# Optimization experiments

Hardware: AMD Instinct MI355X
Metric: run time of the kernel (lower is better)

The kernel has to match this reference:

```python
import jax, jax.numpy as jnp
import numpy as np

N = 50000; E = 1000000; H = 64; HEADS = 4; D = 16; IN = 8; ED = 4; B = 512; EMB = 128; L = 3


def _ln(x, g, b, eps=1e-5):
    mu = jnp.mean(x, axis=-1, keepdims=True)
    var = jnp.mean((x - mu) ** 2, axis=-1, keepdims=True)
    return (x - mu) / jnp.sqrt(var + eps) * g + b


def setup_inputs() -> dict:
    key = jax.random.key(0)
    ks = jax.random.split(key, 24)
    rn = lambda k, s, sc=0.05: jax.random.normal(k, s, jnp.float32) * sc
    return {
        'x': rn(ks[0], (N, IN), 1.0),
        'edge_attr': rn(ks[1], (E, ED), 1.0),
        'edge_index': jax.random.randint(ks[2], (2, E), 0, N),
        'batch': jnp.sort(jax.random.randint(ks[3], (N,), 0, B)),
        'W_in': rn(ks[4], (IN, H)), 'b_in': jnp.zeros(H, jnp.float32),
        'ln1_g': jnp.ones((L, H), jnp.float32), 'ln1_b': jnp.zeros((L, H), jnp.float32),
        'Wq': rn(ks[5], (L, H, H)), 'bq': jnp.zeros((L, H), jnp.float32),
        'Wk': rn(ks[6], (L, H, H)), 'bk': jnp.zeros((L, H), jnp.float32),
        'Wv': rn(ks[7], (L, H, H)), 'bv': jnp.zeros((L, H), jnp.float32),
        'We': rn(ks[8], (L, ED, H)),
        'Wskip': rn(ks[9], (L, H, H)), 'bskip': jnp.zeros((L, H), jnp.float32),
        'Wbeta': rn(ks[10], (L, 3 * H, 1)),
        'ln2_g': jnp.ones((L, H), jnp.float32), 'ln2_b': jnp.zeros((L, H), jnp.float32),
        'W1': rn(ks[11], (L, H, 2 * H)), 'b1': jnp.zeros((L, 2 * H), jnp.float32),
        'W2': rn(ks[12], (L, 2 * H, H)), 'b2': jnp.zeros((L, H), jnp.float32),
        'Wo1': rn(ks[13], (H, EMB)), 'bo1': jnp.zeros(EMB, jnp.float32),
        'Wo2': rn(ks[14], (EMB, EMB)), 'bo2': jnp.zeros(EMB, jnp.float32),
    }


def _forward(x, edge_attr, edge_index, batch, W_in, b_in, ln1_g, ln1_b, Wq, bq, Wk, bk, Wv, bv,
             We, Wskip, bskip, Wbeta, ln2_g, ln2_b, W1, b1, W2, b2, Wo1, bo1, Wo2, bo2):
    src, dst = edge_index[0], edge_index[1]  # message j->i aggregated at dst
    scale = 1.0 / jnp.sqrt(jnp.float32(D))
    x = x @ W_in + b_in  # [N,H]
    for l in range(L):
        xin = x
        h = _ln(x, ln1_g[l], ln1_b[l])
        q = (h @ Wq[l] + bq[l]).reshape(N, HEADS, D)
        k = (h @ Wk[l] + bk[l]).reshape(N, HEADS, D)
        v = (h @ Wv[l] + bv[l]).reshape(N, HEADS, D)
        e = (edge_attr @ We[l]).reshape(E, HEADS, D)
        k_e = k[src] + e  # [E,heads,D]
        v_e = v[src] + e
        s = jnp.sum(q[dst] * k_e, axis=-1) * scale  # [E,heads]
        m = jax.ops.segment_max(s, dst, num_segments=N)  # scatter-softmax max
        m = jnp.where(jnp.isfinite(m), m, 0.0)
        p = jnp.exp(s - m[dst])
        denom = jax.ops.segment_sum(p, dst, num_segments=N)
        alpha = p / (denom[dst] + 1e-16)
        out = jax.ops.segment_sum(alpha[:, :, None] * v_e, dst, num_segments=N).reshape(N, H)
        x_r = h @ Wskip[l] + bskip[l]
        beta = jax.nn.sigmoid(jnp.concatenate([out, x_r, out - x_r], axis=-1) @ Wbeta[l])
        out = beta * x_r + (1.0 - beta) * out
        x = xin + out  # dropout disabled (eval)
        xin = x
        h = _ln(x, ln2_g[l], ln2_b[l])
        h = jax.nn.gelu(h @ W1[l] + b1[l], approximate=False) @ W2[l] + b2[l]
        x = xin + h
    pooled = jax.ops.segment_max(x, batch, num_segments=B)  # global_max_pool
    pooled = jnp.where(jnp.isfinite(pooled), pooled, 0.0)
    emb = jax.nn.relu(pooled @ Wo1 + bo1) @ Wo2 + bo2
    norm = jnp.sqrt(jnp.sum(emb * emb, axis=-1, keepdims=True))
    return emb / jnp.maximum(norm, 1e-12)


def reference(x, edge_attr, edge_index, batch, W_in, b_in, ln1_g, ln1_b, Wq, bq, Wk, bk, Wv, bv,
              We, Wskip, bskip, Wbeta, ln2_g, ln2_b, W1, b1, W2, b2, Wo1, bo1, Wo2, bo2):
    return _forward(x, edge_attr, edge_index, batch, W_in, b_in, ln1_g, ln1_b, Wq, bq, Wk, bk,
                    Wv, bv, We, Wskip, bskip, Wbeta, ln2_g, ln2_b, W1, b1, W2, b2, Wo1, bo1, Wo2, bo2)
```

## Files before the change

kernel.cpp:

```cpp
#include <hip/hip_runtime.h>
#include <hip/hip_bf16.h>
#include <hip/hip_fp16.h>

#define Nn 50000
#define Ee 1000000
#define Bb 512
#define NG 3125
#define SCB 196

typedef unsigned short u16;
typedef unsigned int u32;
typedef _Float16 f16;
typedef _Float16 f16x8 __attribute__((ext_vector_type(8)));
typedef float f32x4 __attribute__((ext_vector_type(4)));

__device__ __forceinline__ u16 f2h(float f) { return __half_as_ushort(__float2half(f)); }
__device__ __forceinline__ float h2f_lo(u32 kv) { return __half2float(__ushort_as_half((u16)(kv & 0xffff))); }
__device__ __forceinline__ float h2f_hi(u32 kv) { return __half2float(__ushort_as_half((u16)(kv >> 16))); }

__device__ __forceinline__ float fexp2(float x) {
    float r;
    asm("v_exp_f32 %0, %1" : "=v"(r) : "v"(x));
    return r;
}

__device__ __forceinline__ float red16(float x) {
    int t;
    t = __builtin_amdgcn_update_dpp(0, __float_as_int(x), 0xB1, 0xF, 0xF, true);
    x += __int_as_float(t);
    t = __builtin_amdgcn_update_dpp(0, __float_as_int(x), 0x4E, 0xF, 0xF, true);
    x += __int_as_float(t);
    t = __builtin_amdgcn_update_dpp(0, __float_as_int(x), 0x141, 0xF, 0xF, true);
    x += __int_as_float(t);
    t = __builtin_amdgcn_update_dpp(0, __float_as_int(x), 0x140, 0xF, 0xF, true);
    x += __int_as_float(t);
    return x;
}

__global__ __launch_bounds__(256) void k_input_proj(const float* __restrict__ x,
    const float* __restrict__ Win, const float* __restrict__ bin, float* __restrict__ X)
{
    __shared__ float W[8][64];
    __shared__ float bsh[64];
    int t = threadIdx.x;
    if (t < 64) bsh[t] = bin[t];
    for (int i = t; i < 512; i += 256) W[i >> 6][i & 63] = Win[i];
    __syncthreads();
    int gid = blockIdx.x * 256 + t;
    int n = gid >> 6, c = gid & 63;
    const float* xr = x + n * 8;
    float acc = bsh[c];
#pragma unroll
    for (int k = 0; k < 8; ++k) acc = fmaf(xr[k], W[k][c], acc);
    X[gid] = acc;
}

__global__ __launch_bounds__(256) void k_hist(const int* __restrict__ ei, int* __restrict__ deg)
{
    int e = blockIdx.x * 256 + threadIdx.x;
    if (e < Ee) atomicAdd(&deg[ei[Ee + e]], 1);
}

__global__ __launch_bounds__(256) void k_part(const int* __restrict__ deg, int* __restrict__ psum)
{
    __shared__ int ws[4];
    int b = blockIdx.x, t = threadIdx.x;
    int idx = b * 256 + t;
    int v = (idx < Nn) ? deg[idx] : 0;
    int r = v;
#pragma unroll
    for (int off = 32; off; off >>= 1) r += __shfl_xor(r, off);
    if ((t & 63) == 0) ws[t >> 6] = r;
    __syncthreads();
    if (t == 0) psum[b] = ws[0] + ws[1] + ws[2] + ws[3];
}

__global__ __launch_bounds__(256) void k_scanp(const int* __restrict__ psum, int* __restrict__ poff)
{
    __shared__ int ws[4];
    int t = threadIdx.x, lane = t & 63, w = t >> 6;
    int v = (t < SCB) ? psum[t] : 0;
    int s = v;
#pragma unroll
    for (int off = 1; off < 64; off <<= 1) {
        int u = __shfl_up(s, off);
        if (lane >= off) s += u;
    }
    if (lane == 63) ws[w] = s;
    __syncthreads();
    if (t == 0) { int a = 0; for (int i = 0; i < 4; ++i) { a += ws[i]; ws[i] = a; } }
    __syncthreads();
    int incl = s + (w ? ws[w - 1] : 0);
    if (t < SCB) poff[t] = incl - v;
}

__global__ __launch_bounds__(256) void k_apply(const int* __restrict__ deg, const int* __restrict__ poff,
    int* __restrict__ rowptr)
{
    __shared__ int ws[4];
    int b = blockIdx.x, t = threadIdx.x, lane = t & 63, w = t >> 6;
    int idx = b * 256 + t;
    int v = (idx < Nn) ? deg[idx] : 0;
    int s = v;
#pragma unroll
    for (int off = 1; off < 64; off <<= 1) {
        int u = __shfl_up(s, off);
        if (lane >= off) s += u;
    }
    if (lane == 63) ws[w] = s;
    __syncthreads();
    if (t == 0) { int a = 0; for (int i = 0; i < 4; ++i) { a += ws[i]; ws[i] = a; } }
    __syncthreads();
    int incl = s + (w ? ws[w - 1] : 0) + poff[b];
    if (idx < Nn) rowptr[idx + 1] = incl;
    if (b == 0 && t == 0) rowptr[0] = 0;
}

__global__ __launch_bounds__(256) void k_scatter(const int* __restrict__ ei, const float* __restrict__ eattr,
    const int* __restrict__ rowptr, int* __restrict__ cursor, int* __restrict__ colsrc,
    float4* __restrict__ ea4)
{
    int e = blockIdx.x * 256 + threadIdx.x;
    if (e >= Ee) return;
    int d = ei[Ee + e];
    int pos = rowptr[d] + atomicAdd(&cursor[d], 1);
    colsrc[pos] = ei[e];
    ea4[pos] = *(const float4*)(eattr + (size_t)e * 4);
}

__device__ __forceinline__ f16x8 load_bfrag(const float* __restrict__ W, int NC, int col, int k0)
{
    f16x8 b;
    const float* wp = W + (size_t)k0 * NC + col;
#pragma unroll
    for (int i = 0; i < 8; ++i) b[i] = (f16)wp[i * NC];
    return b;
}

__device__ __forceinline__ void build_ln_a(const float* __restrict__ X, int n0, int lane,
    const float* __restrict__ lng, const float* __restrict__ lnb, f16x8* a)
{
    const int r = lane & 15, c = lane >> 4;
    const float* xp = X + (size_t)(n0 + r) * 64 + c * 8;
    float4 x0 = *(const float4*)(xp);
    float4 x1 = *(const float4*)(xp + 4);
    float4 x2 = *(const float4*)(xp + 32);
    float4 x3 = *(const float4*)(xp + 36);
    float xs[16] = {x0.x, x0.y, x0.z, x0.w, x1.x, x1.y, x1.z, x1.w,
                    x2.x, x2.y, x2.z, x2.w, x3.x, x3.y, x3.z, x3.w};
    float s = 0.f, s2 = 0.f;
#pragma unroll
    for (int i = 0; i < 16; ++i) { s += xs[i]; s2 = fmaf(xs[i], xs[i], s2); }
    s += __shfl_xor(s, 16);  s += __shfl_xor(s, 32);
    s2 += __shfl_xor(s2, 16); s2 += __shfl_xor(s2, 32);
    float mu = s * 0.015625f;
    float var = s2 * 0.015625f - mu * mu;
    float rstd = rsqrtf(fmaxf(var, 0.f) + 1e-5f);
    const float* gp = lng + c * 8;
    const float* bp = lnb + c * 8;
    float4 g0 = *(const float4*)(gp),      g1 = *(const float4*)(gp + 4);
    float4 g2 = *(const float4*)(gp + 32), g3 = *(const float4*)(gp + 36);
    float4 b0 = *(const float4*)(bp),      b1 = *(const float4*)(bp + 4);
    float4 b2 = *(const float4*)(bp + 32), b3 = *(const float4*)(bp + 36);
    float gs[16] = {g0.x, g0.y, g0.z, g0.w, g1.x, g1.y, g1.z, g1.w,
                    g2.x, g2.y, g2.z, g2.w, g3.x, g3.y, g3.z, g3.w};
    float bs[16] = {b0.x, b0.y, b0.z, b0.w, b1.x, b1.y, b1.z, b1.w,
                    b2.x, b2.y, b2.z, b2.w, b3.x, b3.y, b3.z, b3.w};
#pragma unroll
    for (int i = 0; i < 16; ++i) {
        float h = (xs[i] - mu) * rstd * gs[i] + bs[i];
        a[i >> 3][i & 7] = (f16)h;
    }
}

__global__ __launch_bounds__(256) void k_proj_kv(const float* __restrict__ X, u32* __restrict__ KV,
    const float* __restrict__ Wk, const float* __restrict__ Wv,
    const float* __restrict__ bk, const float* __restrict__ bv,
    const float* __restrict__ lng, const float* __restrict__ lnb)
{
    const int lane = threadIdx.x & 63;
    const int wid = (blockIdx.x * 256 + threadIdx.x) >> 6;
    const int nw = gridDim.x * 4;
    const int ch_base = lane & 15;
    const int k0b = (lane >> 4) * 8;
    f16x8 bw[8][2];
#pragma unroll
    for (int t = 0; t < 4; ++t)
#pragma unroll
        for (int s = 0; s < 2; ++s) {
            bw[t][s]     = load_bfrag(Wk, 64, t * 16 + ch_base, s * 32 + k0b);
            bw[t + 4][s] = load_bfrag(Wv, 64, t * 16 + ch_base, s * 32 + k0b);
        }
    float bk_l[4], bv_l[4];
#pragma unroll
    for (int t = 0; t < 4; ++t) { bk_l[t] = bk[t * 16 + ch_base]; bv_l[t] = bv[t * 16 + ch_base]; }
    for (int g = wid; g < NG; g += nw) {
        int n0 = g * 16;
        f16x8 a[2];
        build_ln_a(X, n0, lane, lng, lnb, a);
        f32x4 acc[8];
#pragma unroll
        for (int t = 0; t < 8; ++t) { acc[t][0] = 0.f; acc[t][1] = 0.f; acc[t][2] = 0.f; acc[t][3] = 0.f; }
#pragma unroll
        for (int t = 0; t < 8; ++t)
#pragma unroll
            for (int s = 0; s < 2; ++s)
                acc[t] = __builtin_amdgcn_mfma_f32_16x16x32_f16(a[s], bw[t][s], acc[t], 0, 0, 0);
        int rbase = n0 + (lane >> 4) * 4;
#pragma unroll
        for (int t = 0; t < 4; ++t) {
            int ch = t * 16 + ch_base;
#pragma unroll
            for (int j = 0; j < 4; ++j) {
                u32 lo = f2h(acc[t][j] + bk_l[t]);
                u32 hi = f2h(acc[t + 4][j] + bv_l[t]);
                KV[(size_t)(rbase + j) * 64 + ch] = (hi << 16) | lo;
            }
        }
    }
}

__global__ __launch_bounds__(256) void k_proj_qs(const float* __restrict__ X, float* __restrict__ QX,
    const float* __restrict__ Wq, const float* __restrict__ Ws,
    const float* __restrict__ bq, const float* __restrict__ bs_,
    const float* __restrict__ lng, const float* __restrict__ lnb)
{
    const int lane = threadIdx.x & 63;
    const int wid = (blockIdx.x * 256 + threadIdx.x) >> 6;
    const int nw = gridDim.x * 4;
    const int ch_base = lane & 15;
    const int k0b = (lane >> 4) * 8;
    f16x8 bw[8][2];
#pragma unroll
    for (int t = 0; t < 4; ++t)
#pragma unroll
        for (int s = 0; s < 2; ++s) {
            bw[t][s]     = load_bfrag(Wq, 64, t * 16 + ch_base, s * 32 + k0b);
            bw[t + 4][s] = load_bfrag(Ws, 64, t * 16 + ch_base, s * 32 + k0b);
        }
    float bq_l[4], bs_l[4];
#pragma unroll
    for (int t = 0; t < 4; ++t) { bq_l[t] = bq[t * 16 + ch_base]; bs_l[t] = bs_[t * 16 + ch_base]; }
    for (int g = wid; g < NG; g += nw) {
        int n0 = g * 16;
        f16x8 a[2];
        build_ln_a(X, n0, lane, lng, lnb, a);
        f32x4 acc[8];
#pragma unroll
        for (int t = 0; t < 8; ++t) { acc[t][0] = 0.f; acc[t][1] = 0.f; acc[t][2] = 0.f; acc[t][3] = 0.f; }
#pragma unroll
        for (int t = 0; t < 8; ++t)
#pragma unroll
            for (int s = 0; s < 2; ++s)
                acc[t] = __builtin_amdgcn_mfma_f32_16x16x32_f16(a[s], bw[t][s], acc[t], 0, 0, 0);
        int rbase = n0 + (lane >> 4) * 4;
#pragma unroll
        for (int t = 0; t < 4; ++t) {
            int ch = t * 16 + ch_base;
#pragma unroll
            for (int j = 0; j < 4; ++j) {
                float* dst = QX + (size_t)(rbase + j) * 128;
                dst[ch] = acc[t][j] + bq_l[t];
                dst[64 + ch] = acc[t + 4][j] + bs_l[t];
            }
        }
    }
}

__global__ __launch_bounds__(256) void k_edge(
    const float* __restrict__ QX, const u32* __restrict__ KV, float* __restrict__ X,
    const int* __restrict__ rowptr, const int* __restrict__ colsrc,
    const float4* __restrict__ ea4,
    const float* __restrict__ We, const float* __restrict__ Wbeta)
{
    const float SCL = 0.25f * 1.4426950408889634f;
    int lane = threadIdx.x & 63;
    int node = blockIdx.x * 4 + (threadIdx.x >> 6);
    if (node >= Nn) return;
    float we0 = We[lane], we1 = We[64 + lane];
    float we2 = We[128 + lane], we3 = We[192 + lane];
    float wbA = Wbeta[lane] + Wbeta[128 + lane];
    float wbB = Wbeta[64 + lane] - Wbeta[128 + lane];
    const float* qrow = QX + (size_t)node * 128;
    float q = qrow[lane] * SCL;
    float xr = qrow[64 + lane];
    int jb = rowptr[node], je = rowptr[node + 1];
    float l0 = 0.f, l1 = 0.f, a0 = 0.f, a1 = 0.f;
    int j = jb;
    for (; j + 3 < je; j += 4) {
        int src[4]; float4 eb[4]; u32 kv[4];
#pragma unroll
        for (int c = 0; c < 4; ++c) src[c] = colsrc[j + c];
#pragma unroll
        for (int c = 0; c < 4; ++c) kv[c] = KV[(src[c] << 6) | lane];
#pragma unroll
        for (int c = 0; c < 4; ++c) eb[c] = ea4[j + c];
        float pe[4], ve[4];
#pragma unroll
        for (int c = 0; c < 4; ++c) {
            float e = we0 * eb[c].x;
            e = fmaf(we1, eb[c].y, e); e = fmaf(we2, eb[c].z, e); e = fmaf(we3, eb[c].w, e);
            float ke = h2f_lo(kv[c]) + e;
            ve[c] = h2f_hi(kv[c]) + e;
            float p = red16(q * ke);
            pe[c] = fexp2(p);
        }
        l0 += pe[0]; l1 += pe[1];
        a0 = fmaf(pe[0], ve[0], a0); a1 = fmaf(pe[1], ve[1], a1);
        l0 += pe[2]; l1 += pe[3];
        a0 = fmaf(pe[2], ve[2], a0); a1 = fmaf(pe[3], ve[3], a1);
    }
    for (; j < je; ++j) {
        int s0 = colsrc[j];
        float4 eb0 = ea4[j];
        u32 kv0 = KV[(s0 << 6) | lane];
        float e0 = we0 * eb0.x;
        e0 = fmaf(we1, eb0.y, e0); e0 = fmaf(we2, eb0.z, e0); e0 = fmaf(we3, eb0.w, e0);
        float ke0 = h2f_lo(kv0) + e0, ve0 = h2f_hi(kv0) + e0;
        float p0 = red16(q * ke0);
        float pe0 = fexp2(p0);
        l0 += pe0;
        a0 = fmaf(pe0, ve0, a0);
    }
    float lsum = l0 + l1;
    float acc = a0 + a1;
    float outv = acc / (lsum + 1e-16f);
    float tb = outv * wbA + xr * wbB;
#pragma unroll
    for (int off = 32; off; off >>= 1) tb += __shfl_xor(tb, off);
    float beta = 1.f / (1.f + __expf(-tb));
    float res = beta * xr + (1.f - beta) * outv;
    X[(size_t)node * 64 + lane] += res;
}

__global__ __launch_bounds__(256) void k_ffn1_m(const float* __restrict__ X, u16* __restrict__ G16,
    const float* __restrict__ W1, const float* __restrict__ b1,
    const float* __restrict__ lng, const float* __restrict__ lnb)
{
    const int lane = threadIdx.x & 63;
    const int wid = (blockIdx.x * 256 + threadIdx.x) >> 6;
    const int nw = gridDim.x * 4;
    const int ch_base = lane & 15;
    const int k0b = (lane >> 4) * 8;
    f16x8 bw[8][2];
#pragma unroll
    for (int t = 0; t < 8; ++t)
#pragma unroll
        for (int s = 0; s < 2; ++s)
            bw[t][s] = load_bfrag(W1, 128, t * 16 + ch_base, s * 32 + k0b);
    float b1_l[8];
#pragma unroll
    for (int t = 0; t < 8; ++t) b1_l[t] = b1[t * 16 + ch_base];
    for (int g = wid; g < NG; g += nw) {
        int n0 = g * 16;
        f16x8 a[2];
        build_ln_a(X, n0, lane, lng, lnb, a);
        f32x4 acc[8];
#pragma unroll
        for (int t = 0; t < 8; ++t) { acc[t][0] = 0.f; acc[t][1] = 0.f; acc[t][2] = 0.f; acc[t][3] = 0.f; }
#pragma unroll
        for (int t = 0; t < 8; ++t)
#pragma unroll
            for (int s = 0; s < 2; ++s)
                acc[t] = __builtin_amdgcn_mfma_f32_16x16x32_f16(a[s], bw[t][s], acc[t], 0, 0, 0);
        int rbase = n0 + (lane >> 4) * 4;
#pragma unroll
        for (int t = 0; t < 8; ++t) {
            int ch = t * 16 + ch_base;
#pragma unroll
            for (int j = 0; j < 4; ++j) {
                float v = acc[t][j] + b1_l[t];
                float o = 0.5f * v * (1.f + erff(v * 0.7071067811865476f));
                G16[(size_t)(rbase + j) * 128 + ch] = f2h(o);
            }
        }
    }
}

__global__ __launch_bounds__(256) void k_ffn2_m(const u16* __restrict__ G16, float* __restrict__ X,
    const float* __restrict__ W2, const float* __restrict__ b2,
    const int* __restrict__ batch, u32* __restrict__ pkeys, int dopool)
{
    const int lane = threadIdx.x & 63;
    const int wid = (blockIdx.x * 256 + threadIdx.x) >> 6;
    const int nw = gridDim.x * 4;
    const int ch_base = lane & 15;
    const int k0b = (lane >> 4) * 8;
    f16x8 bw[4][4];
#pragma unroll
    for (int t = 0; t < 4; ++t)
#pragma unroll
        for (int s = 0; s < 4; ++s)
            bw[t][s] = load_bfrag(W2, 64, t * 16 + ch_base, s * 32 + k0b);
    float b2_l[4];
#pragma unroll
    for (int t = 0; t < 4; ++t) b2_l[t] = b2[t * 16 + ch_base];
    for (int g = wid; g < NG; g += nw) {
        int n0 = g * 16;
        const u16* gp = G16 + (size_t)(n0 + ch_base) * 128 + k0b;
        f16x8 a0 = *(const f16x8*)(gp);
        f16x8 a1 = *(const f16x8*)(gp + 32);
        f16x8 a2 = *(const f16x8*)(gp + 64);
        f16x8 a3 = *(const f16x8*)(gp + 96);
        f32x4 acc[4];
#pragma unroll
        for (int t = 0; t < 4; ++t) { acc[t][0] = 0.f; acc[t][1] = 0.f; acc[t][2] = 0.f; acc[t][3] = 0.f; }
#pragma unroll
        for (int t = 0; t < 4; ++t) {
            acc[t] = __builtin_amdgcn_mfma_f32_16x16x32_f16(a0, bw[t][0], acc[t], 0, 0, 0);
            acc[t] = __builtin_amdgcn_mfma_f32_16x16x32_f16(a1, bw[t][1], acc[t], 0, 0, 0);
            acc[t] = __builtin_amdgcn_mfma_f32_16x16x32_f16(a2, bw[t][2], acc[t], 0, 0, 0);
            acc[t] = __builtin_amdgcn_mfma_f32_16x16x32_f16(a3, bw[t][3], acc[t], 0, 0, 0);
        }
        int rbase = n0 + (lane >> 4) * 4;
#pragma unroll
        for (int t = 0; t < 4; ++t) {
            int ch = t * 16 + ch_base;
#pragma unroll
            for (int j = 0; j < 4; ++j) {
                int n = rbase + j;
                float* dst = X + (size_t)n * 64 + ch;
                float v = *dst + acc[t][j] + b2_l[t];
                *dst = v;
                if (dopool) {
                    u32 u = __float_as_uint(v);
                    u32 key = (u >> 31) ? ~u : (u | 0x80000000u);
                    atomicMax(&pkeys[batch[n] * 64 + ch], key);
                }
            }
        }
    }
}

__global__ __launch_bounds__(128) void k_head(const u32* __restrict__ pkeys,
    const float* __restrict__ Wo1, const float* __restrict__ bo1,
    const float* __restrict__ Wo2, const float* __restrict__ bo2,
    float* __restrict__ out)
{
    __shared__ float P[64];
    __shared__ float E1[128];
    __shared__ float wred[2];
    int b = blockIdx.x, t = threadIdx.x;
    if (t < 64) {
        u32 k = pkeys[b * 64 + t];
        float v = 0.f;
        if (k) v = (k >> 31) ? __uint_as_float(k ^ 0x80000000u) : __uint_as_float(~k);
        P[t] = v;
    }
    __syncthreads();
    float a = bo1[t];
#pragma unroll 8
    for (int k = 0; k < 64; ++k) a = fmaf(P[k], Wo1[k * 128 + t], a);
    E1[t] = fmaxf(a, 0.f);
    __syncthreads();
    float o = bo2[t];
#pragma unroll 8
    for (int k = 0; k < 128; ++k) o = fmaf(E1[k], Wo2[k * 128 + t], o);
    float ss = o * o;
#pragma unroll
    for (int off = 32; off; off >>= 1) ss += __shfl_xor(ss, off);
    if ((t & 63) == 0) wred[t >> 6] = ss;
    __syncthreads();
    float tot = wred[0] + wred[1];
    float nrm = fmaxf(sqrtf(tot), 1e-12f);
    out[b * 128 + t] = o / nrm;
}

extern "C" void kernel_launch(void* const* d_in, const int* in_sizes, int n_in,
                              void* d_out, int out_size, void* d_ws, size_t ws_size,
                              hipStream_t stream)
{
    const float* x         = (const float*)d_in[0];
    const float* edge_attr = (const float*)d_in[1];
    const int* ei          = (const int*)d_in[2];
    const int* batch       = (const int*)d_in[3];
    const float* Win  = (const float*)d_in[4];
    const float* bin  = (const float*)d_in[5];
    const float* ln1g = (const float*)d_in[6];
    const float* ln1b = (const float*)d_in[7];
    const float* Wq   = (const float*)d_in[8];
    const float* bq   = (const float*)d_in[9];
    const float* Wk   = (const float*)d_in[10];
    const float* bk   = (const float*)d_in[11];
    const float* Wv   = (const float*)d_in[12];
    const float* bv   = (const float*)d_in[13];
    const float* We   = (const float*)d_in[14];
    const float* Wsk  = (const float*)d_in[15];
    const float* bsk  = (const float*)d_in[16];
    const float* Wbe  = (const float*)d_in[17];
    const float* ln2g = (const float*)d_in[18];
    const float* ln2b = (const float*)d_in[19];
    const float* W1   = (const float*)d_in[20];
    const float* b1   = (const float*)d_in[21];
    const float* W2   = (const float*)d_in[22];
    const float* b2   = (const float*)d_in[23];
    const float* Wo1  = (const float*)d_in[24];
    const float* bo1  = (const float*)d_in[25];
    const float* Wo2  = (const float*)d_in[26];
    const float* bo2  = (const float*)d_in[27];

    char* wsp = (char*)d_ws;
    size_t off = 0;
    auto alloc = [&](size_t bytes) { void* p = wsp + off; off = (off + bytes + 255) & ~(size_t)255; return p; };
    float*   X      = (float*)alloc((size_t)Nn * 64 * 4);
    float*   QX     = (float*)alloc((size_t)Nn * 128 * 4);
    u32*     KV     = (u32*)alloc((size_t)Nn * 64 * 4);
    u16*     G16    = (u16*)alloc((size_t)Nn * 128 * 2);
    int*     rowptr = (int*)alloc((size_t)(Nn + 1) * 4);
    int*     deg    = (int*)alloc((size_t)Nn * 4);
    int*     cursor = (int*)alloc((size_t)Nn * 4);
    int*     psum   = (int*)alloc((size_t)SCB * 4);
    int*     poff   = (int*)alloc((size_t)SCB * 4);
    int*     colsrc = (int*)alloc((size_t)Ee * 4);
    float4*  ea4    = (float4*)alloc((size_t)Ee * 16);
    u32*     pkeys  = (u32*)alloc((size_t)Bb * 64 * 4);

    hipMemsetAsync(deg, 0, (size_t)Nn * 4, stream);
    hipMemsetAsync(cursor, 0, (size_t)Nn * 4, stream);
    hipMemsetAsync(pkeys, 0, (size_t)Bb * 64 * 4, stream);

    k_input_proj<<<12500, 256, 0, stream>>>(x, Win, bin, X);
    k_hist<<<(Ee + 255) / 256, 256, 0, stream>>>(ei, deg);
    k_part<<<SCB, 256, 0, stream>>>(deg, psum);
    k_scanp<<<1, 256, 0, stream>>>(psum, poff);
    k_apply<<<SCB, 256, 0, stream>>>(deg, poff, rowptr);
    k_scatter<<<(Ee + 255) / 256, 256, 0, stream>>>(ei, edge_attr, rowptr, cursor, colsrc, ea4);

    const int GB = 512;
    for (int l = 0; l < 3; ++l) {
        k_proj_kv<<<GB, 256, 0, stream>>>(X, KV, Wk + l * 4096, Wv + l * 4096,
            bk + l * 64, bv + l * 64, ln1g + l * 64, ln1b + l * 64);
        k_proj_qs<<<GB, 256, 0, stream>>>(X, QX, Wq + l * 4096, Wsk + l * 4096,
            bq + l * 64, bsk + l * 64, ln1g + l * 64, ln1b + l * 64);
        k_edge<<<Nn / 4, 256, 0, stream>>>(QX, KV, X, rowptr, colsrc, ea4,
            We + l * 256, Wbe + l * 192);
        k_ffn1_m<<<GB, 256, 0, stream>>>(X, G16, W1 + l * 8192, b1 + l * 128,
            ln2g + l * 64, ln2b + l * 64);
        k_ffn2_m<<<GB, 256, 0, stream>>>(G16, X, W2 + l * 8192, b2 + l * 64,
            batch, pkeys, (l == 2) ? 1 : 0);
    }
    k_head<<<Bb, 128, 0, stream>>>(pkeys, Wo1, bo1, Wo2, bo2, (float*)d_out);
}
```

Measured before the change: 479.7 us.

## Fuse Q/skip with K/V projections and the two FFN matmuls via LDS

Merges the two projection kernels into one, so LayerNorm and the X read happen once per node tile for all four projections. Fuses FFN1 and FFN2 into one kernel: the GELU output tile goes to per-wave LDS and is consumed there, removing the global G16 buffer and its write/read round trip. This cuts two launches per layer. In exchange, weight fragments are reloaded inside the tile loop instead of once per wave, raising register and cache pressure; the FFN kernel also passes X as both restrict input and output.

```diff
diff --git a/kernel.cpp b/kernel.cpp
--- a/kernel.cpp
+++ b/kernel.cpp
@@ -173,8 +173,11 @@
     }
 }
 
-__global__ __launch_bounds__(256) void k_proj_kv(const float* __restrict__ X, u32* __restrict__ KV,
+__global__ __launch_bounds__(256) void k_proj(const float* __restrict__ X,
+    float* __restrict__ QX, u32* __restrict__ KV,
+    const float* __restrict__ Wq, const float* __restrict__ Ws,
     const float* __restrict__ Wk, const float* __restrict__ Wv,
+    const float* __restrict__ bq, const float* __restrict__ bs_,
     const float* __restrict__ bk, const float* __restrict__ bv,
     const float* __restrict__ lng, const float* __restrict__ lnb)
 {
@@ -183,85 +186,71 @@
     const int nw = gridDim.x * 4;
     const int ch_base = lane & 15;
     const int k0b = (lane >> 4) * 8;
-    f16x8 bw[8][2];
-#pragma unroll
-    for (int t = 0; t < 4; ++t)
-#pragma unroll
-        for (int s = 0; s < 2; ++s) {
-            bw[t][s]     = load_bfrag(Wk, 64, t * 16 + ch_base, s * 32 + k0b);
-            bw[t + 4][s] = load_bfrag(Wv, 64, t * 16 + ch_base, s * 32 + k0b);
-        }
-    float bk_l[4], bv_l[4];
-#pragma unroll
-    for (int t = 0; t < 4; ++t) { bk_l[t] = bk[t * 16 + ch_base]; bv_l[t] = bv[t * 16 + ch_base]; }
+    float bq_l[4], bs_l[4], bk_l[4], bv_l[4];
+#pragma unroll
+    for (int t = 0; t < 4; ++t) {
+        bq_l[t] = bq[t * 16 + ch_base]; bs_l[t] = bs_[t * 16 + ch_base];
+        bk_l[t] = bk[t * 16 + ch_base]; bv_l[t] = bv[t * 16 + ch_base];
+    }
     for (int g = wid; g < NG; g += nw) {
         int n0 = g * 16;
         f16x8 a[2];
         build_ln_a(X, n0, lane, lng, lnb, a);
-        f32x4 acc[8];
-#pragma unroll
-        for (int t = 0; t < 8; ++t) { acc[t][0] = 0.f; acc[t][1] = 0.f; acc[t][2] = 0.f; acc[t][3] = 0.f; }
-#pragma unroll
-        for (int t = 0; t < 8; ++t)
-#pragma unroll
-            for (int s = 0; s < 2; ++s)
-                acc[t] = __builtin_amdgcn_mfma_f32_16x16x32_f16(a[s], bw[t][s], acc[t], 0, 0, 0);
         int rbase = n0 + (lane >> 4) * 4;
-#pragma unroll
-        for (int t = 0; t < 4; ++t) {
-            int ch = t * 16 + ch_base;
-#pragma unroll
-            for (int j = 0; j < 4; ++j) {
-                u32 lo = f2h(acc[t][j] + bk_l[t]);
-                u32 hi = f2h(acc[t + 4][j] + bv_l[t]);
-                KV[(size_t)(rbase + j) * 64 + ch] = (hi << 16) | lo;
+        {
+            f16x8 bw[8][2];
+#pragma unroll
+            for (int t = 0; t < 4; ++t)
+#pragma unroll
+                for (int s = 0; s < 2; ++s) {
+                    bw[t][s]     = load_bfrag(Wq, 64, t * 16 + ch_base, s * 32 + k0b);
+                    bw[t + 4][s] = load_bfrag(Ws, 64, t * 16 + ch_base, s * 32 + k0b);
+                }
+            f32x4 acc[8];
+#pragma unroll
+            for (int t = 0; t < 8; ++t) { acc[t][0] = 0.f; acc[t][1] = 0.f; acc[t][2] = 0.f; acc[t][3] = 0.f; }
+#pragma unroll
+            for (int t = 0; t < 8; ++t)
+#pragma unroll
+                for (int s = 0; s < 2; ++s)
+                    acc[t] = __builtin_amdgcn_mfma_f32_16x16x32_f16(a[s], bw[t][s], acc[t], 0, 0, 0);
+#pragma unroll
+            for (int t = 0; t < 4; ++t) {
+                int ch = t * 16 + ch_base;
+#pragma unroll
+                for (int j = 0; j < 4; ++j) {
+                    float* dst = QX + (size_t)(rbase + j) * 128;
+                    dst[ch] = acc[t][j] + bq_l[t];
+                    dst[64 + ch] = acc[t + 4][j] + bs_l[t];
+                }
             }
         }
-    }
-}
-
-__global__ __launch_bounds__(256) void k_proj_qs(const float* __restrict__ X, float* __restrict__ QX,
-    const float* __restrict__ Wq, const float* __restrict__ Ws,
-    const float* __restrict__ bq, const float* __restrict__ bs_,
-    const float* __restrict__ lng, const float* __restrict__ lnb)
-{
-    const int lane = threadIdx.x & 63;
-    const int wid = (blockIdx.x * 256 + threadIdx.x) >> 6;
-    const int nw = gridDim.x * 4;
-    const int ch_base = lane & 15;
-    const int k0b = (lane >> 4) * 8;
-    f16x8 bw[8][2];
-#pragma unroll
-    for (int t = 0; t < 4; ++t)
-#pragma unroll
-        for (int s = 0; s < 2; ++s) {
-            bw[t][s]     = load_bfrag(Wq, 64, t * 16 + ch_base, s * 32 + k0b);
-            bw[t + 4][s] = load_bfrag(Ws, 64, t * 16 + ch_base, s * 32 + k0b);
-        }
-    float bq_l[4], bs_l[4];
-#pragma unroll
-    for (int t = 0; t < 4; ++t) { bq_l[t] = bq[t * 16 + ch_base]; bs_l[t] = bs_[t * 16 + ch_base]; }
-    for (int g = wid; g < NG; g += nw) {
-        int n0 = g * 16;
-        f16x8 a[2];
-        build_ln_a(X, n0, lane, lng, lnb, a);
-        f32x4 acc[8];
-#pragma unroll
-        for (int t = 0; t < 8; ++t) { acc[t][0] = 0.f; acc[t][1] = 0.f; acc[t][2] = 0.f; acc[t][3] = 0.f; }
-#pragma unroll
-        for (int t = 0; t < 8; ++t)
-#pragma unroll
-            for (int s = 0; s < 2; ++s)
-                acc[t] = __builtin_amdgcn_mfma_f32_16x16x32_f16(a[s], bw[t][s], acc[t], 0, 0, 0);
-        int rbase = n0 + (lane >> 4) * 4;
-#pragma unroll
-        for (int t = 0; t < 4; ++t) {
-            int ch = t * 16 + ch_base;
-#pragma unroll
-            for (int j = 0; j < 4; ++j) {
-                float* dst = QX + (size_t)(rbase + j) * 128;
-                dst[ch] = acc[t][j] + bq_l[t];
-                dst[64 + ch] = acc[t + 4][j] + bs_l[t];
+        {
+            f16x8 bw[8][2];
+#pragma unroll
+            for (int t = 0; t < 4; ++t)
+#pragma unroll
+                for (int s = 0; s < 2; ++s) {
+                    bw[t][s]     = load_bfrag(Wk, 64, t * 16 + ch_base, s * 32 + k0b);
+                    bw[t + 4][s] = load_bfrag(Wv, 64, t * 16 + ch_base, s * 32 + k0b);
+                }
+            f32x4 acc[8];
+#pragma unroll
+            for (int t = 0; t < 8; ++t) { acc[t][0] = 0.f; acc[t][1] = 0.f; acc[t][2] = 0.f; acc[t][3] = 0.f; }
+#pragma unroll
+            for (int t = 0; t < 8; ++t)
+#pragma unroll
+                for (int s = 0; s < 2; ++s)
+                    acc[t] = __builtin_amdgcn_mfma_f32_16x16x32_f16(a[s], bw[t][s], acc[t], 0, 0, 0);
+#pragma unroll
+            for (int t = 0; t < 4; ++t) {
+                int ch = t * 16 + ch_base;
+#pragma unroll
+                for (int j = 0; j < 4; ++j) {
+                    u32 lo = f2h(acc[t][j] + bk_l[t]);
+                    u32 hi = f2h(acc[t + 4][j] + bv_l[t]);
+                    KV[(size_t)(rbase + j) * 64 + ch] = (hi << 16) | lo;
+                }
             }
         }
     }
@@ -333,99 +322,90 @@
     X[(size_t)node * 64 + lane] += res;
 }
 
-__global__ __launch_bounds__(256) void k_ffn1_m(const float* __restrict__ X, u16* __restrict__ G16,
+__global__ __launch_bounds__(256) void k_ffn(const float* __restrict__ X_in, float* __restrict__ X,
     const float* __restrict__ W1, const float* __restrict__ b1,
-    const float* __restrict__ lng, const float* __restrict__ lnb)
-{
+    const float* __restrict__ W2, const float* __restrict__ b2,
+    const float* __restrict__ lng, const float* __restrict__ lnb,
+    const int* __restrict__ batch, u32* __restrict__ pkeys, int dopool)
+{
+    __shared__ u16 lds[4][16][136];
     const int lane = threadIdx.x & 63;
+    const int wloc = threadIdx.x >> 6;
     const int wid = (blockIdx.x * 256 + threadIdx.x) >> 6;
     const int nw = gridDim.x * 4;
     const int ch_base = lane & 15;
     const int k0b = (lane >> 4) * 8;
-    f16x8 bw[8][2];
-#pragma unroll
-    for (int t = 0; t < 8; ++t)
-#pragma unroll
-        for (int s = 0; s < 2; ++s)
-            bw[t][s] = load_bfrag(W1, 128, t * 16 + ch_base, s * 32 + k0b);
     float b1_l[8];
 #pragma unroll
     for (int t = 0; t < 8; ++t) b1_l[t] = b1[t * 16 + ch_base];
+    float b2_l[4];
+#pragma unroll
+    for (int t = 0; t < 4; ++t) b2_l[t] = b2[t * 16 + ch_base];
     for (int g = wid; g < NG; g += nw) {
         int n0 = g * 16;
         f16x8 a[2];
-        build_ln_a(X, n0, lane, lng, lnb, a);
-        f32x4 acc[8];
-#pragma unroll
-        for (int t = 0; t < 8; ++t) { acc[t][0] = 0.f; acc[t][1] = 0.f; acc[t][2] = 0.f; acc[t][3] = 0.f; }
-#pragma unroll
-        for (int t = 0; t < 8; ++t)
-#pragma unroll
-            for (int s = 0; s < 2; ++s)
-                acc[t] = __builtin_amdgcn_mfma_f32_16x16x32_f16(a[s], bw[t][s], acc[t], 0, 0, 0);
+        build_ln_a(X_in, n0, lane, lng, lnb, a);
         int rbase = n0 + (lane >> 4) * 4;
-#pragma unroll
-        for (int t = 0; t < 8; ++t) {
-            int ch = t * 16 + ch_base;
-#pragma unroll
-            for (int j = 0; j < 4; ++j) {
-                float v = acc[t][j] + b1_l[t];
-                float o = 0.5f * v * (1.f + erff(v * 0.7071067811865476f));
-                G16[(size_t)(rbase + j) * 128 + ch] = f2h(o);
+        {
+            f16x8 bw[8][2];
+#pragma unroll
+            for (int t = 0; t < 8; ++t)
+#pragma unroll
+                for (int s = 0; s < 2; ++s)
+                    bw[t][s] = load_bfrag(W1, 128, t * 16 + ch_base, s * 32 + k0b);
+            f32x4 acc[8];
+#pragma unroll
+            for (int t = 0; t < 8; ++t) { acc[t][0] = 0.f; acc[t][1] = 0.f; acc[t][2] = 0.f; acc[t][3] = 0.f; }
+#pragma unroll
+            for (int t = 0; t < 8; ++t)
+#pragma unroll
+                for (int s = 0; s < 2; ++s)
+                    acc[t] = __builtin_amdgcn_mfma_f32_16x16x32_f16(a[s], bw[t][s], acc[t], 0, 0, 0);
+            const int rloc = (lane >> 4) * 4;
+#pragma unroll
+            for (int t = 0; t < 8; ++t) {
+                int ch = t * 16 + ch_base;
+#pragma unroll
+                for (int j = 0; j < 4; ++j) {
+                    float v = acc[t][j] + b1_l[t];
+                    float o = 0.5f * v * (1.f + erff(v * 0.7071067811865476f));
+                    lds[wloc][rloc + j][ch] = f2h(o);
+                }
             }
         }
-    }
-}
-
-__global__ __launch_bounds__(256) void k_ffn2_m(const u16* __restrict__ G16, float* __restrict__ X,
-    const float* __restrict__ W2, const float* __restrict__ b2,
-    const int* __restrict__ batch, u32* __restrict__ pkeys, int dopool)
-{
-    const int lane = threadIdx.x & 63;
-    const int wid = (blockIdx.x * 256 + threadIdx.x) >> 6;
-    const int nw = gridDim.x * 4;
-    const int ch_base = lane & 15;
-    const int k0b = (lane >> 4) * 8;
-    f16x8 bw[4][4];
-#pragma unroll
-    for (int t = 0; t < 4; ++t)
-#pragma unroll
-        for (int s = 0; s < 4; ++s)
-            bw[t][s] = load_bfrag(W2, 64, t * 16 + ch_base, s * 32 + k0b);
-    float b2_l[4];
-#pragma unroll
-    for (int t = 0; t < 4; ++t) b2_l[t] = b2[t * 16 + ch_base];
-    for (int g = wid; g < NG; g += nw) {
-        int n0 = g * 16;
-        const u16* gp = G16 + (size_t)(n0 + ch_base) * 128 + k0b;
-        f16x8 a0 = *(const f16x8*)(gp);
-        f16x8 a1 = *(const f16x8*)(gp + 32);
-        f16x8 a2 = *(const f16x8*)(gp + 64);
-        f16x8 a3 = *(const f16x8*)(gp + 96);
-        f32x4 acc[4];
-#pragma unroll
-        for (int t = 0; t < 4; ++t) { acc[t][0] = 0.f; acc[t][1] = 0.f; acc[t][2] = 0.f; acc[t][3] = 0.f; }
-#pragma unroll
-        for (int t = 0; t < 4; ++t) {
-            acc[t] = __builtin_amdgcn_mfma_f32_16x16x32_f16(a0, bw[t][0], acc[t], 0, 0, 0);
-            acc[t] = __builtin_amdgcn_mfma_f32_16x16x32_f16(a1, bw[t][1], acc[t], 0, 0, 0);
-            acc[t] = __builtin_amdgcn_mfma_f32_16x16x32_f16(a2, bw[t][2], acc[t], 0, 0, 0);
-            acc[t] = __builtin_amdgcn_mfma_f32_16x16x32_f16(a3, bw[t][3], acc[t], 0, 0, 0);
-        }
-        int rbase = n0 + (lane >> 4) * 4;
-#pragma unroll
-        for (int t = 0; t < 4; ++t) {
-            int ch = t * 16 + ch_base;
-#pragma unroll
-            for (int j = 0; j < 4; ++j) {
-                int n = rbase + j;
-                float* dst = X + (size_t)n * 64 + ch;
-                float v = *dst + acc[t][j] + b2_l[t];
-                *dst = v;
-                if (dopool) {
-                    u32 u = __float_as_uint(v);
-                    u32 key = (u >> 31) ? ~u : (u | 0x80000000u);
-                    atomicMax(&pkeys[batch[n] * 64 + ch], key);
+        {
+            f16x8 ga[4];
+#pragma unroll
+            for (int s = 0; s < 4; ++s)
+                ga[s] = *(const f16x8*)&lds[wloc][ch_base][s * 32 + k0b];
+            f16x8 bw[4][4];
+#pragma unroll
+            for (int t = 0; t < 4; ++t)
+#pragma unroll
+                for (int s = 0; s < 4; ++s)
+                    bw[t][s] = load_bfrag(W2, 64, t * 16 + ch_base, s * 32 + k0b);
+            f32x4 acc[4];
+#pragma unroll
+            for (int t = 0; t < 4; ++t) { acc[t][0] = 0.f; acc[t][1] = 0.f; acc[t][2] = 0.f; acc[t][3] = 0.f; }
+#pragma unroll
+            for (int t = 0; t < 4; ++t)
+#pragma unroll
+                for (int s = 0; s < 4; ++s)
+                    acc[t] = __builtin_amdgcn_mfma_f32_16x16x32_f16(ga[s], bw[t][s], acc[t], 0, 0, 0);
+#pragma unroll
+            for (int t = 0; t < 4; ++t) {
+                int ch = t * 16 + ch_base;
+#pragma unroll
+                for (int j = 0; j < 4; ++j) {
+                    int n = rbase + j;
+                    float* dst = X + (size_t)n * 64 + ch;
+                    float v = *dst + acc[t][j] + b2_l[t];
+                    *dst = v;
+                    if (dopool) {
+                        u32 u = __float_as_uint(v);
+                        u32 key = (u >> 31) ? ~u : (u | 0x80000000u);
+                        atomicMax(&pkeys[batch[n] * 64 + ch], key);
+                    }
                 }
             }
         }
@@ -505,7 +485,6 @@
     float*   X      = (float*)alloc((size_t)Nn * 64 * 4);
     float*   QX     = (float*)alloc((size_t)Nn * 128 * 4);
     u32*     KV     = (u32*)alloc((size_t)Nn * 64 * 4);
-    u16*     G16    = (u16*)alloc((size_t)Nn * 128 * 2);
     int*     rowptr = (int*)alloc((size_t)(Nn + 1) * 4);
     int*     deg    = (int*)alloc((size_t)Nn * 4);
     int*     cursor = (int*)alloc((size_t)Nn * 4);
@@ -528,15 +507,14 @@
 
     const int GB = 512;
     for (int l = 0; l < 3; ++l) {
-        k_proj_kv<<<GB, 256, 0, stream>>>(X, KV, Wk + l * 4096, Wv + l * 4096,
-            bk + l * 64, bv + l * 64, ln1g + l * 64, ln1b + l * 64);
-        k_proj_qs<<<GB, 256, 0, stream>>>(X, QX, Wq + l * 4096, Wsk + l * 4096,
-            bq + l * 64, bsk + l * 64, ln1g + l * 64, ln1b + l * 64);
+        k_proj<<<GB, 256, 0, stream>>>(X, QX, KV,
+            Wq + l * 4096, Wsk + l * 4096, Wk + l * 4096, Wv + l * 4096,
+            bq + l * 64, bsk + l * 64, bk + l * 64, bv + l * 64,
+            ln1g + l * 64, ln1b + l * 64);
         k_edge<<<Nn / 4, 256, 0, stream>>>(QX, KV, X, rowptr, colsrc, ea4,
             We + l * 256, Wbe + l * 192);
-        k_ffn1_m<<<GB, 256, 0, stream>>>(X, G16, W1 + l * 8192, b1 + l * 128,
-            ln2g + l * 64, ln2b + l * 64);
-        k_ffn2_m<<<GB, 256, 0, stream>>>(G16, X, W2 + l * 8192, b2 + l * 64,
+        k_ffn<<<GB, 256, 0, stream>>>(X, X, W1 + l * 8192, b1 + l * 128,
+            W2 + l * 8192, b2 + l * 64, ln2g + l * 64, ln2b + l * 64,
             batch, pkeys, (l == 2) ? 1 : 0);
     }
     k_head<<<Bb, 128, 0, stream>>>(pkeys, Wo1, bo1, Wo2, bo2, (float*)d_out);
```

New measurement: 494.0 us. +3.0%, slower.
